# Optimization experiments

Hardware: AMD Instinct MI355X
Metric: run time of the kernel (lower is better)

The kernel has to match this reference:

```python
import jax, jax.numpy as jnp
import numpy as np

NUM_CLASSES = 250
NUM_EMB = 128
EMB_DIM = 512
HID = 256
IN_DIM = 225
COMMIT = 0.25


def _lstm_dir(x, Wih, Whh, b, reverse):
    # x: [B, T, D]; Wih: [4H, D]; Whh: [4H, H]; b: [4H]
    B = x.shape[0]
    H = Whh.shape[1]
    xs = jnp.swapaxes(x, 0, 1)            # [T, B, D]
    pre = xs @ Wih.T + b                   # precompute input projection: [T, B, 4H]

    def step(carry, pre_t):
        h, c = carry
        g = pre_t + h @ Whh.T
        i, f, gg, o = jnp.split(g, 4, axis=-1)  # torch gate order i,f,g,o
        i = jax.nn.sigmoid(i)
        f = jax.nn.sigmoid(f)
        gg = jnp.tanh(gg)
        o = jax.nn.sigmoid(o)
        c = f * c + i * gg
        h = o * jnp.tanh(c)
        return (h, c), h

    init = (jnp.zeros((B, H), x.dtype), jnp.zeros((B, H), x.dtype))
    _, hs = jax.lax.scan(step, init, pre, reverse=reverse)
    return jnp.swapaxes(hs, 0, 1)          # [B, T, H]


def _bilstm(x, Wih_f, Whh_f, b_f, Wih_b, Whh_b, b_b):
    hf = _lstm_dir(x, Wih_f, Whh_f, b_f, reverse=False)
    hb = _lstm_dir(x, Wih_b, Whh_b, b_b, reverse=True)
    return jnp.concatenate([hf, hb], axis=-1)  # [B, T, 2H]


def _vq(z, codebook):
    flat = z.reshape(-1, codebook.shape[1])  # [N, E]
    d = (jnp.sum(flat ** 2, axis=1, keepdims=True)
         + jnp.sum(codebook ** 2, axis=1)
         - 2.0 * flat @ codebook.T)          # [N, K]
    idx = jnp.argmin(d, axis=1)              # [N]
    q = codebook[idx].reshape(z.shape)
    e_loss = jnp.mean((jax.lax.stop_gradient(q) - z) ** 2)
    q_loss = jnp.mean((q - jax.lax.stop_gradient(z)) ** 2)
    loss = q_loss + COMMIT * e_loss
    q_st = z + jax.lax.stop_gradient(q - z)  # straight-through
    return q_st, loss


def setup_inputs() -> dict:
    key = jax.random.key(0)
    ks = jax.random.split(key, 16)
    s = 0.05
    d = {
        'x': jax.random.normal(ks[0], (64, 512, IN_DIM), dtype=jnp.float32),
        'enc_Wih_f': jax.random.normal(ks[1], (4 * HID, IN_DIM), jnp.float32) * s,
        'enc_Whh_f': jax.random.normal(ks[2], (4 * HID, HID), jnp.float32) * s,
        'enc_b_f': jnp.zeros((4 * HID,), jnp.float32),
        'enc_Wih_b': jax.random.normal(ks[3], (4 * HID, IN_DIM), jnp.float32) * s,
        'enc_Whh_b': jax.random.normal(ks[4], (4 * HID, HID), jnp.float32) * s,
        'enc_b_b': jnp.zeros((4 * HID,), jnp.float32),
        'codebook': jax.random.uniform(ks[5], (NUM_EMB, EMB_DIM), jnp.float32,
                                       minval=-1.0 / NUM_EMB, maxval=1.0 / NUM_EMB),
        'dec_Wih_f': jax.random.normal(ks[6], (4 * HID, EMB_DIM), jnp.float32) * s,
        'dec_Whh_f': jax.random.normal(ks[7], (4 * HID, HID), jnp.float32) * s,
        'dec_b_f': jnp.zeros((4 * HID,), jnp.float32),
        'dec_Wih_b': jax.random.normal(ks[8], (4 * HID, EMB_DIM), jnp.float32) * s,
        'dec_Whh_b': jax.random.normal(ks[9], (4 * HID, HID), jnp.float32) * s,
        'dec_b_b': jnp.zeros((4 * HID,), jnp.float32),
        'W_cls': jax.random.normal(ks[10], (NUM_CLASSES, EMB_DIM), jnp.float32) * s,
        'b_cls': jnp.zeros((NUM_CLASSES,), jnp.float32),
    }
    return d


def reference(x, enc_Wih_f, enc_Whh_f, enc_b_f, enc_Wih_b, enc_Whh_b, enc_b_b,
              codebook, dec_Wih_f, dec_Whh_f, dec_b_f, dec_Wih_b, dec_Whh_b, dec_b_b,
              W_cls, b_cls):
    enc_out = _bilstm(x, enc_Wih_f, enc_Whh_f, enc_b_f, enc_Wih_b, enc_Whh_b, enc_b_b)  # [B,T,512]
    quantized, vq_loss = _vq(enc_out, codebook)
    dec_out = _bilstm(quantized, dec_Wih_f, dec_Whh_f, dec_b_f, dec_Wih_b, dec_Whh_b, dec_b_b)
    logits = dec_out[:, -1] @ W_cls.T + b_cls  # [B, num_classes]
    return logits, vq_loss
```

## Files before the change

### kernel.cpp

```cpp
#include <hip/hip_runtime.h>
#include <hip/hip_fp16.h>
#include <cstddef>

#define Bb 64
#define Tt 512
#define INRAW 225
#define Hh 256
#define G4 1024
#define Ee 512
#define NCODE 128
#define NCLS 250

typedef _Float16 half8_t __attribute__((ext_vector_type(8)));
typedef float f32x4 __attribute__((ext_vector_type(4)));
typedef unsigned u32x4 __attribute__((ext_vector_type(4)));

__device__ __forceinline__ float sigf(float x) { return 1.0f / (1.0f + expf(-x)); }
__device__ __forceinline__ float fsig(float x) { return __builtin_amdgcn_rcpf(1.0f + __expf(-x)); }
__device__ __forceinline__ float ftanh(float x) {
  return 2.0f * __builtin_amdgcn_rcpf(1.0f + __expf(-2.0f * x)) - 1.0f;
}

__device__ __forceinline__ unsigned pkmax16(unsigned a, unsigned b) {
  unsigned r;
  asm("v_pk_max_i16 %0, %1, %2" : "=v"(r) : "v"(a), "v"(b));
  return r;
}

__global__ __launch_bounds__(256) void prep_all_k(
    u32x4* __restrict__ hexfill, const float* __restrict__ x, _Float16* __restrict__ xh,
    const float* __restrict__ dWihB, float* __restrict__ wpkbd,
    const float* __restrict__ eWhhF, _Float16* __restrict__ wphF,
    const float* __restrict__ eWhhB, _Float16* __restrict__ wphB,
    const float* __restrict__ dWhhF, _Float16* __restrict__ wphD,
    const float* __restrict__ eWihF, _Float16* __restrict__ wpihF,
    const float* __restrict__ eWihB, _Float16* __restrict__ wpihB,
    const float* __restrict__ dWihF, _Float16* __restrict__ wpihD) {
  int blk = blockIdx.x;
  const int tid = threadIdx.x;

  if (blk < 24576) {
    long i = (long)blk * 256 + tid;
    u32x4 v = {0x7C007C00u, 0x7C007C00u, 0x7C007C00u, 0x7C007C00u};
    asm volatile("global_store_dwordx4 %0, %1, off sc0 sc1"
                 :: "v"(hexfill + i), "v"(v) : "memory");
    return;
  }
  blk -= 24576;
  if (blk < 32768) {
    int idx = blk * 256 + tid;
    int row = idx >> 8, k = idx & 255;
    xh[idx] = (k < INRAW) ? (_Float16)x[(size_t)row * INRAW + k] : (_Float16)0.f;
    return;
  }
  blk -= 32768;
  if (blk < 2048) {
    int idx = blk * 256 + tid;
    int jg = idx >> 9;
    int k = idx & 511;
    int j = jg >> 2, g = jg & 3;
    wpkbd[(((size_t)k << 8) + j) * 4 + g] = dWihB[(size_t)(g * 256 + j) * 512 + k];
    return;
  }
  blk -= 2048;
  if (blk < 3072) {
    const float* W = (blk < 1024) ? eWhhF : (blk < 2048) ? eWhhB : dWhhF;
    _Float16* wp = (blk < 1024) ? wphF : (blk < 2048) ? wphB : wphD;
    int idx = (blk & 1023) * 256 + tid;
    int e = idx & 7, l = (idx >> 3) & 63, zg = (idx >> 9) & 7;
    int ks = (idx >> 12) & 7, wv = (idx >> 15) & 7;
    int z = zg >> 2, g = zg & 3;
    int u = wv * 32 + z * 16 + (l & 15);
    int k = ks * 32 + (l >> 4) * 8 + e;
    wp[idx] = (_Float16)W[(size_t)(g * 256 + u) * 256 + k];
    return;
  }
  blk -= 3072;
  if (blk < 2048) {
    const float* W = (blk < 1024) ? eWihF : eWihB;
    _Float16* wp = (blk < 1024) ? wpihF : wpihB;
    int idx = (blk & 1023) * 256 + tid;
    int e = idx & 7, l = (idx >> 3) & 63;
    int tail = idx >> 9;
    int ks = tail & 7; tail >>= 3;
    int z = tail & 1, w = (tail >> 1) & 7, g = tail >> 4;
    if (g >= 4) return;
    int k = ks * 32 + (l >> 4) * 8 + e;
    int u = w * 32 + z * 16 + (l & 15);
    wp[idx] = (k < INRAW) ? (_Float16)W[(size_t)(g * 256 + u) * INRAW + k] : (_Float16)0.f;
    return;
  }
  blk -= 2048;
  {
    int idx = blk * 256 + tid;
    int e = idx & 7, l = (idx >> 3) & 63;
    int tail = idx >> 9;
    int ks = tail & 15; tail >>= 4;
    int z = tail & 1, w = (tail >> 1) & 7, g = tail >> 4;
    if (g >= 4) return;
    int k = ks * 32 + (l >> 4) * 8 + e;
    int u = w * 32 + z * 16 + (l & 15);
    wpihD[idx] = (_Float16)dWihF[(size_t)(g * 256 + u) * 512 + k];
  }
}

__global__ __launch_bounds__(256) void gemm_mfma_pre(const _Float16* __restrict__ Ah,
                                                     const _Float16* __restrict__ Bp0,
                                                     const float* __restrict__ bias0,
                                                     __half* __restrict__ C0,
                                                     const _Float16* __restrict__ Bp1,
                                                     const float* __restrict__ bias1,
                                                     __half* __restrict__ C1, int K) {
  const int t = blockIdx.x, g = blockIdx.y;
  const int zsel = blockIdx.z;
  const _Float16* Bp = zsel ? Bp1 : Bp0;
  const float* bias = zsel ? bias1 : bias0;
  __half* C = zsel ? C1 : C0;
  const int bg = threadIdx.x >> 6;
  const int l = threadIdx.x & 63, l15 = l & 15, lg = l >> 4;
  const int KS = K >> 5;

  f32x4 acc[16];
#pragma unroll
  for (int ct = 0; ct < 16; ++ct) acc[ct] = (f32x4){0.f, 0.f, 0.f, 0.f};

  const _Float16* arow = Ah + ((size_t)(bg * 16 + l15) * 512 + t) * K + lg * 8;

  for (int kh = 0; kh < KS; kh += 8) {
    half8_t af[8];
#pragma unroll
    for (int k2 = 0; k2 < 8; ++k2)
      af[k2] = *(const half8_t*)(arow + (kh + k2) * 32);
#pragma unroll
    for (int ct = 0; ct < 16; ++ct) {
      const int w = ct >> 1, z = ct & 1;
      const _Float16* bb = Bp + ((((size_t)(g * 8 + w) * 2 + z) * KS + kh) * 64 + l) * 8;
#pragma unroll
      for (int k2 = 0; k2 < 8; ++k2) {
        half8_t bf = *(const half8_t*)(bb + (size_t)k2 * 512);
        acc[ct] = __builtin_amdgcn_mfma_f32_16x16x32_f16(af[k2], bf, acc[ct], 0, 0, 0);
      }
    }
  }

#pragma unroll
  for (int ct = 0; ct < 16; ++ct) {
    const int w = ct >> 1, z = ct & 1;
    const int u = w * 32 + z * 16 + l15;
    const float bs = bias[g * 256 + u];
    union { unsigned short us[4]; uint2 u2; } pk;
#pragma unroll
    for (int j = 0; j < 4; ++j) {
      __half hv = __float2half(acc[ct][j] + bs);
      pk.us[j] = *(unsigned short*)&hv;
    }
    __half* dst = C + ((((size_t)t * 4 + bg) * 8 + w) * 2 + z) * 1024 + l * 16 + g * 4;
    *(uint2*)dst = pk.u2;
  }
}

__global__ __launch_bounds__(64) void lstm_scan_sync(
    const half8_t* __restrict__ preF, const half8_t* __restrict__ wF,
    _Float16* __restrict__ hexF,
    const half8_t* __restrict__ preB, const half8_t* __restrict__ wB,
    _Float16* __restrict__ hexB, int nfwd) {
  const int isB = (blockIdx.x >= nfwd) ? 1 : 0;
  const half8_t* pre = isB ? preB : preF;
  const half8_t* wfrag = isB ? wB : wF;
  _Float16* hex = isB ? hexB : hexF;
  const int bid = blockIdx.x - (isB ? nfwd : 0);
  const int rg = bid >> 4, sl = bid & 15;
  const int w_ = sl >> 1, z_ = sl & 1;
  const int l = threadIdx.x, l15 = l & 15, lg = l >> 4;
  const int u0 = sl * 16;

  half8_t bfr[8][4];
#pragma unroll
  for (int ks = 0; ks < 8; ++ks)
#pragma unroll
    for (int g = 0; g < 4; ++g)
      bfr[ks][g] = wfrag[(size_t)((w_ * 8 + ks) * 8 + z_ * 4 + g) * 64 + l];

  float c[4] = {0.f, 0.f, 0.f, 0.f};
  half8_t pc0, pc1;
  {
    const int t0 = isB ? (Tt - 1) : 0;
    const half8_t* pp = pre + ((size_t)(t0 * 4 + rg) * 16 + sl) * 128 + l * 2;
    pc0 = pp[0]; pc1 = pp[1];
  }

  for (int s = 0; s < Tt; ++s) {
    f32x4 acc[4];
#pragma unroll
    for (int g = 0; g < 4; ++g)
#pragma unroll
      for (int j = 0; j < 4; ++j)
        acc[g][j] = (float)((g < 2 ? pc0 : pc1)[(g & 1) * 4 + j]);

    if (s + 1 < Tt) {
      const int tn = isB ? (Tt - 2 - s) : (s + 1);
      const half8_t* pp = pre + ((size_t)(tn * 4 + rg) * 16 + sl) * 128 + l * 2;
      pc0 = pp[0]; pc1 = pp[1];
    }

    if (s > 0) {
      const char* ab = (const char*)hex + (((size_t)(s - 1) * 64 + rg * 16) * 256) * 2;
      half8_t afr[8];
      while (true) {
#pragma unroll
        for (int ks = 0; ks < 8; ++ks) {
          const void* ap = (const void*)(ab + l15 * 512 + ks * 64 + lg * 16);
          asm volatile("global_load_dwordx4 %0, %1, off sc0 sc1"
                       : "=v"(afr[ks]) : "v"(ap) : "memory");
        }
        asm volatile("s_waitcnt vmcnt(0)" ::: "memory");
        union HU { half8_t h; u32x4 u; } cu;
        cu.h = afr[0];
        unsigned mm = pkmax16(pkmax16(cu.u[0], cu.u[1]), pkmax16(cu.u[2], cu.u[3]));
#pragma unroll
        for (int ks = 1; ks < 8; ++ks) {
          cu.h = afr[ks];
          mm = pkmax16(mm, pkmax16(pkmax16(cu.u[0], cu.u[1]), pkmax16(cu.u[2], cu.u[3])));
        }
        int bad = ((mm & 0xFFFFu) == 0x7C00u) || ((mm >> 16) == 0x7C00u);
        if (__all(!bad)) break;
      }
      __builtin_amdgcn_sched_barrier(0);

#pragma unroll
      for (int ks = 0; ks < 8; ++ks)
#pragma unroll
        for (int g = 0; g < 4; ++g)
          acc[g] = __builtin_amdgcn_mfma_f32_16x16x32_f16(afr[ks], bfr[ks][g], acc[g], 0, 0, 0);
    }

#pragma unroll
    for (int j = 0; j < 4; ++j) {
      float iv = fsig(acc[0][j]);
      float fv = fsig(acc[1][j]);
      float gv = ftanh(acc[2][j]);
      float ov = fsig(acc[3][j]);
      c[j] = fv * c[j] + iv * gv;
      float hv = ov * ftanh(c[j]);
      union { _Float16 f; unsigned short u; } cv;
      cv.f = (_Float16)hv;
      unsigned hb32 = cv.u;
      const void* hp = (const void*)(hex + ((size_t)s * 64 + rg * 16 + lg * 4 + j) * 256
                                     + u0 + l15);
      asm volatile("global_store_short %0, %1, off sc0 sc1"
                   :: "v"(hp), "v"(hb32) : "memory");
    }
  }
}

#define VPB 4
__global__ __launch_bounds__(128) void vq_kernel(const _Float16* __restrict__ hexF,
                                                 const _Float16* __restrict__ hexB,
                                                 const float* __restrict__ cb,
                                                 _Float16* __restrict__ qh,
                                                 float* __restrict__ dmin) {
  const int tid = threadIdx.x;
  const int v0 = blockIdx.x * VPB;
  __shared__ __align__(16) float zs[VPB][Ee];
  __shared__ float dsh[NCODE];
  __shared__ int ish[NCODE];
  __shared__ int best[VPB];

#pragma unroll
  for (int v = 0; v < VPB; ++v) {
    const int vv = v0 + v;
    const int b = vv >> 9, t = vv & 511;
    const _Float16* hf = hexF + ((size_t)t * 64 + b) * 256;
    const _Float16* hb = hexB + ((size_t)(Tt - 1 - t) * 64 + b) * 256;
    zs[v][tid]       = (float)hf[tid];
    zs[v][tid + 128] = (float)hf[tid + 128];
    zs[v][tid + 256] = (float)hb[tid];
    zs[v][tid + 384] = (float)hb[tid + 128];
  }
  __syncthreads();

  float dv[VPB] = {0.0f, 0.0f, 0.0f, 0.0f};
  const float4* crow = (const float4*)(cb + (size_t)tid * Ee);
#pragma unroll 2
  for (int e4 = 0; e4 < Ee / 4; ++e4) {
    float4 cc = crow[e4];
#pragma unroll
    for (int v = 0; v < VPB; ++v) {
      float4 z = *(const float4*)&zs[v][e4 * 4];
      float t0 = z.x - cc.x, t1 = z.y - cc.y, t2 = z.z - cc.z, t3 = z.w - cc.w;
      dv[v] = fmaf(t0, t0, dv[v]);
      dv[v] = fmaf(t1, t1, dv[v]);
      dv[v] = fmaf(t2, t2, dv[v]);
      dv[v] = fmaf(t3, t3, dv[v]);
    }
  }

#pragma unroll
  for (int v = 0; v < VPB; ++v) {
    __syncthreads();
    dsh[tid] = dv[v];
    ish[tid] = tid;
    __syncthreads();
    for (int off = 64; off > 0; off >>= 1) {
      if (tid < off) {
        float dn = dsh[tid + off];
        int in_ = ish[tid + off];
        if (dn < dsh[tid] || (dn == dsh[tid] && in_ < ish[tid])) {
          dsh[tid] = dn;
          ish[tid] = in_;
        }
      }
      __syncthreads();
    }
    if (tid == 0) {
      best[v] = ish[0];
      dmin[v0 + v] = dsh[0];
    }
  }
  __syncthreads();

#pragma unroll
  for (int v = 0; v < VPB; ++v) {
    const float* cbest = cb + (size_t)best[v] * Ee;
    _Float16* qrow = qh + (size_t)(v0 + v) * Ee;
#pragma unroll
    for (int u = 0; u < 4; ++u) {
      int e = tid + u * 128;
      float z = zs[v][e];
      qrow[e] = (_Float16)(z + (cbest[e] - z));
    }
  }
}

__global__ __launch_bounds__(1024) void vq_reduce(const float* __restrict__ dmin,
                                                  float* __restrict__ out) {
  __shared__ float sh[1024];
  int tid = threadIdx.x;
  float s = 0.0f;
  for (int i = tid; i < Bb * Tt; i += 1024) s += dmin[i];
  sh[tid] = s;
  __syncthreads();
  for (int off = 512; off > 0; off >>= 1) {
    if (tid < off) sh[tid] += sh[tid + off];
    __syncthreads();
  }
  if (tid == 0) out[Bb * NCLS] = sh[0] * (1.25f / ((float)(Bb * Tt) * (float)Ee));
}

__global__ __launch_bounds__(256) void dec_bwd_last(const _Float16* __restrict__ qh,
                                                    const float* __restrict__ wpB,
                                                    const float* __restrict__ bias,
                                                    float* __restrict__ hb_last) {
  int b = blockIdx.x, tid = threadIdx.x;
  __shared__ __align__(16) float zsl[Ee];
  const _Float16* qrow = qh + ((size_t)b * Tt + (Tt - 1)) * Ee;
  zsl[tid] = (float)qrow[tid];
  zsl[tid + 256] = (float)qrow[tid + 256];
  __syncthreads();
  float a0 = bias[tid], a1 = bias[256 + tid], a2 = bias[512 + tid], a3 = bias[768 + tid];
  const float4* wp4 = (const float4*)wpB;
#pragma unroll 4
  for (int k = 0; k < Ee; ++k) {
    float zk = zsl[k];
    float4 w = wp4[((size_t)k << 8) + tid];
    a0 = fmaf(zk, w.x, a0); a1 = fmaf(zk, w.y, a1);
    a2 = fmaf(zk, w.z, a2); a3 = fmaf(zk, w.w, a3);
  }
  float i = sigf(a0), f = sigf(a1), g = tanhf(a2), o = sigf(a3);
  (void)f;
  float cc = i * g;
  hb_last[b * Hh + tid] = o * tanhf(cc);
}

__global__ __launch_bounds__(256) void classifier_k(const _Float16* __restrict__ hexD,
                                                    const float* __restrict__ hb_last,
                                                    const float* __restrict__ Wcls,
                                                    const float* __restrict__ bcls,
                                                    float* __restrict__ out) {
  int b = blockIdx.x, tid = threadIdx.x;
  __shared__ __align__(16) float dl[Ee];
  dl[tid] = (float)hexD[((size_t)(Tt - 1) * 64 + b) * 256 + tid];
  dl[tid + 256] = hb_last[b * Hh + tid];
  __syncthreads();
  if (tid < NCLS) {
    const float4* wr = (const float4*)(Wcls + (size_t)tid * Ee);
    float acc = bcls[tid];
#pragma unroll 4
    for (int e4 = 0; e4 < Ee / 4; ++e4) {
      float4 w = wr[e4];
      float4 z = *(const float4*)&dl[e4 * 4];
      acc = fmaf(w.x, z.x, acc);
      acc = fmaf(w.y, z.y, acc);
      acc = fmaf(w.z, z.z, acc);
      acc = fmaf(w.w, z.w, acc);
    }
    out[b * NCLS + tid] = acc;
  }
}

extern "C" void kernel_launch(void* const* d_in, const int* in_sizes, int n_in,
                              void* d_out, int out_size, void* d_ws, size_t ws_size,
                              hipStream_t stream) {
  const float* x     = (const float*)d_in[0];
  const float* eWihF = (const float*)d_in[1];
  const float* eWhhF = (const float*)d_in[2];
  const float* ebF   = (const float*)d_in[3];
  const float* eWihB = (const float*)d_in[4];
  const float* eWhhB = (const float*)d_in[5];
  const float* ebB   = (const float*)d_in[6];
  const float* cb    = (const float*)d_in[7];
  const float* dWihF = (const float*)d_in[8];
  const float* dWhhF = (const float*)d_in[9];
  const float* dbF   = (const float*)d_in[10];
  const float* dWihB = (const float*)d_in[11];
  const float* dbB   = (const float*)d_in[13];
  const float* Wcls  = (const float*)d_in[14];
  const float* bcls  = (const float*)d_in[15];
  float* out = (float*)d_out;
  float* w = (float*)d_ws;

  const size_t MR = (size_t)Bb * Tt;
  const size_t SZ_PRE_H = MR * G4 / 2;
  const size_t SZ_HEX  = (size_t)Tt * Bb * Hh / 2;
  const size_t SZ_XH   = MR * 256 / 2;
  const size_t SZ_WPK  = (size_t)512 * G4;
  const size_t SZ_WPH  = (size_t)G4 * Hh / 2;
  const size_t SZ_WIH  = (size_t)4 * 8 * 2 * 8 * 64 * 8 / 2;
  const size_t SZ_WIHD = SZ_WIH * 2;

  size_t o = 0;
  __half* preFh = (__half*)(w + o); o += SZ_PRE_H;
  __half* preBh = (__half*)(w + o); o += SZ_PRE_H;
  _Float16* hexF = (_Float16*)(w + o); o += SZ_HEX;
  _Float16* hexB = (_Float16*)(w + o); o += SZ_HEX;
  _Float16* hexD = (_Float16*)(w + o); o += SZ_HEX;
  _Float16* xh = (_Float16*)(w + o); o += SZ_XH;
  float* wpkbd = w + o; o += SZ_WPK;
  _Float16* wphF = (_Float16*)(w + o); o += SZ_WPH;
  _Float16* wphB = (_Float16*)(w + o); o += SZ_WPH;
  _Float16* wphD = (_Float16*)(w + o); o += SZ_WPH;
  _Float16* wpihF = (_Float16*)(w + o); o += SZ_WIH;
  _Float16* wpihB = (_Float16*)(w + o); o += SZ_WIH;
  _Float16* wpihD = (_Float16*)(w + o); o += SZ_WIHD;
  float* dminp = w + o; o += MR;
  float* hbl   = w + o; o += (size_t)Bb * Hh;
  _Float16* qh = (_Float16*)preFh;
  __half* dprf = preBh;

  hipLaunchKernelGGL(prep_all_k, dim3(66560), dim3(256), 0, stream,
                     (u32x4*)hexF, x, xh,
                     dWihB, wpkbd,
                     eWhhF, wphF, eWhhB, wphB, dWhhF, wphD,
                     eWihF, wpihF, eWihB, wpihB, dWihF, wpihD);

  hipLaunchKernelGGL(gemm_mfma_pre, dim3(Tt, 4, 2), dim3(256), 0, stream,
                     xh, wpihF, ebF, preFh, wpihB, ebB, preBh, 256);

  hipLaunchKernelGGL(lstm_scan_sync, dim3(128), dim3(64), 0, stream,
                     (const half8_t*)preFh, (const half8_t*)wphF, hexF,
                     (const half8_t*)preBh, (const half8_t*)wphB, hexB, 64);

  hipLaunchKernelGGL(vq_kernel, dim3((int)(MR / VPB)), dim3(128), 0, stream,
                     hexF, hexB, cb, qh, dminp);
  hipLaunchKernelGGL(vq_reduce, dim3(1), dim3(1024), 0, stream, dminp, out);

  hipLaunchKernelGGL(gemm_mfma_pre, dim3(Tt, 4, 1), dim3(256), 0, stream,
                     qh, wpihD, dbF, dprf, wpihD, dbF, dprf, 512);

  hipLaunchKernelGGL(dec_bwd_last, dim3(Bb), dim3(256), 0, stream, qh, wpkbd, dbB, hbl);

  hipLaunchKernelGGL(lstm_scan_sync, dim3(64), dim3(64), 0, stream,
                     (const half8_t*)dprf, (const half8_t*)wphD, hexD,
                     (const half8_t*)dprf, (const half8_t*)wphD, hexD, 64);

  hipLaunchKernelGGL(classifier_k, dim3(Bb), dim3(256), 0, stream,
                     hexD, hbl, Wcls, bcls, out);
}
```

Baseline: 2.545 ms.

## Poll local L2 mirror for LSTM hidden-state exchange with system-scope fallback

The recurrent scan now writes each hidden state twice: to an L2-scoped buffer (sc0 only) and to the coherent global buffer (sc0 sc1). Consumers poll the cheaper L2-scoped copy a few times before falling back to the fully coherent copy. Blocks are remapped so the eight row groups of one slice are interleaved by blockIdx, which is intended to place cooperating blocks on the same XCD and L2. The cost is extra stores, extra inf-fill kernels for the mirror buffers, and reliance on an assumed block-to-XCD placement.

Result: slower. 2.863 ms (+12.5%).

```diff
diff --git a/kernel.cpp b/kernel.cpp
--- a/kernel.cpp
+++ b/kernel.cpp
@@ -27,8 +27,18 @@
   return r;
 }
 
+__global__ __launch_bounds__(256) void fill_inf4_k(u32x4* __restrict__ p, long n4) {
+  long i = (long)blockIdx.x * 256 + threadIdx.x;
+  const long stride = (long)gridDim.x * 256;
+  u32x4 v = {0x7C007C00u, 0x7C007C00u, 0x7C007C00u, 0x7C007C00u};
+  for (; i < n4; i += stride) {
+    asm volatile("global_store_dwordx4 %0, %1, off sc0 sc1" :: "v"(p + i), "v"(v) : "memory");
+  }
+}
+
 __global__ __launch_bounds__(256) void prep_all_k(
-    u32x4* __restrict__ hexfill, const float* __restrict__ x, _Float16* __restrict__ xh,
+    u32x4* __restrict__ hexfill, u32x4* __restrict__ hexblfill,
+    const float* __restrict__ x, _Float16* __restrict__ xh,
     const float* __restrict__ dWihB, float* __restrict__ wpkbd,
     const float* __restrict__ eWhhF, _Float16* __restrict__ wphF,
     const float* __restrict__ eWhhB, _Float16* __restrict__ wphB,
@@ -38,15 +48,22 @@
     const float* __restrict__ dWihF, _Float16* __restrict__ wpihD) {
   int blk = blockIdx.x;
   const int tid = threadIdx.x;
-
-  if (blk < 24576) {
+  u32x4 sv = {0x7C007C00u, 0x7C007C00u, 0x7C007C00u, 0x7C007C00u};
+
+  if (blk < 12288) {
     long i = (long)blk * 256 + tid;
-    u32x4 v = {0x7C007C00u, 0x7C007C00u, 0x7C007C00u, 0x7C007C00u};
     asm volatile("global_store_dwordx4 %0, %1, off sc0 sc1"
-                 :: "v"(hexfill + i), "v"(v) : "memory");
+                 :: "v"(hexfill + i), "v"(sv) : "memory");
     return;
   }
-  blk -= 24576;
+  blk -= 12288;
+  if (blk < 4096) {
+    long i = (long)blk * 256 + tid;
+    asm volatile("global_store_dwordx4 %0, %1, off sc0 sc1"
+                 :: "v"(hexblfill + i), "v"(sv) : "memory");
+    return;
+  }
+  blk -= 4096;
   if (blk < 32768) {
     int idx = blk * 256 + tid;
     int row = idx >> 8, k = idx & 255;
@@ -161,15 +178,19 @@
 
 __global__ __launch_bounds__(64) void lstm_scan_sync(
     const half8_t* __restrict__ preF, const half8_t* __restrict__ wF,
-    _Float16* __restrict__ hexF,
+    _Float16* __restrict__ hexgF, _Float16* __restrict__ hexlF,
     const half8_t* __restrict__ preB, const half8_t* __restrict__ wB,
-    _Float16* __restrict__ hexB, int nfwd) {
-  const int isB = (blockIdx.x >= nfwd) ? 1 : 0;
+    _Float16* __restrict__ hexgB, _Float16* __restrict__ hexlB,
+    int ngTot) {
+  const int group = blockIdx.x & 7;
+  const int sl = blockIdx.x >> 3;
+  if (group >= ngTot) return;
+  const int isB = (group >= 4) ? 1 : 0;
+  const int rg = group & 3;
   const half8_t* pre = isB ? preB : preF;
   const half8_t* wfrag = isB ? wB : wF;
-  _Float16* hex = isB ? hexB : hexF;
-  const int bid = blockIdx.x - (isB ? nfwd : 0);
-  const int rg = bid >> 4, sl = bid & 15;
+  _Float16* hexg = isB ? hexgB : hexgF;
+  _Float16* hexl = isB ? hexlB : hexlF;
   const int w_ = sl >> 1, z_ = sl & 1;
   const int l = threadIdx.x, l15 = l & 15, lg = l >> 4;
   const int u0 = sl * 16;
@@ -204,13 +225,16 @@
     }
 
     if (s > 0) {
-      const char* ab = (const char*)hex + (((size_t)(s - 1) * 64 + rg * 16) * 256) * 2;
+      const size_t boff = (((size_t)(s - 1) * 64 + rg * 16) * 256) * 2;
+      const char* abl = (const char*)hexl + boff;
+      const char* abg = (const char*)hexg + boff;
       half8_t afr[8];
-      while (true) {
+      int ok = 0;
+      for (int tr = 0; tr < 4; ++tr) {
 #pragma unroll
         for (int ks = 0; ks < 8; ++ks) {
-          const void* ap = (const void*)(ab + l15 * 512 + ks * 64 + lg * 16);
-          asm volatile("global_load_dwordx4 %0, %1, off sc0 sc1"
+          const void* ap = (const void*)(abl + l15 * 512 + ks * 64 + lg * 16);
+          asm volatile("global_load_dwordx4 %0, %1, off sc0"
                        : "=v"(afr[ks]) : "v"(ap) : "memory");
         }
         asm volatile("s_waitcnt vmcnt(0)" ::: "memory");
@@ -223,7 +247,28 @@
           mm = pkmax16(mm, pkmax16(pkmax16(cu.u[0], cu.u[1]), pkmax16(cu.u[2], cu.u[3])));
         }
         int bad = ((mm & 0xFFFFu) == 0x7C00u) || ((mm >> 16) == 0x7C00u);
-        if (__all(!bad)) break;
+        if (__all(!bad)) { ok = 1; break; }
+      }
+      if (!ok) {
+        while (true) {
+#pragma unroll
+          for (int ks = 0; ks < 8; ++ks) {
+            const void* ap = (const void*)(abg + l15 * 512 + ks * 64 + lg * 16);
+            asm volatile("global_load_dwordx4 %0, %1, off sc0 sc1"
+                         : "=v"(afr[ks]) : "v"(ap) : "memory");
+          }
+          asm volatile("s_waitcnt vmcnt(0)" ::: "memory");
+          union HU { half8_t h; u32x4 u; } cu;
+          cu.h = afr[0];
+          unsigned mm = pkmax16(pkmax16(cu.u[0], cu.u[1]), pkmax16(cu.u[2], cu.u[3]));
+#pragma unroll
+          for (int ks = 1; ks < 8; ++ks) {
+            cu.h = afr[ks];
+            mm = pkmax16(mm, pkmax16(pkmax16(cu.u[0], cu.u[1]), pkmax16(cu.u[2], cu.u[3])));
+          }
+          int bad = ((mm & 0xFFFFu) == 0x7C00u) || ((mm >> 16) == 0x7C00u);
+          if (__all(!bad)) break;
+        }
       }
       __builtin_amdgcn_sched_barrier(0);
 
@@ -245,10 +290,11 @@
       union { _Float16 f; unsigned short u; } cv;
       cv.f = (_Float16)hv;
       unsigned hb32 = cv.u;
-      const void* hp = (const void*)(hex + ((size_t)s * 64 + rg * 16 + lg * 4 + j) * 256
-                                     + u0 + l15);
+      const size_t hidx = ((size_t)s * 64 + rg * 16 + lg * 4 + j) * 256 + u0 + l15;
+      asm volatile("global_store_short %0, %1, off sc0"
+                   :: "v"((const void*)(hexl + hidx)), "v"(hb32) : "memory");
       asm volatile("global_store_short %0, %1, off sc0 sc1"
-                   :: "v"(hp), "v"(hb32) : "memory");
+                   :: "v"((const void*)(hexg + hidx)), "v"(hb32) : "memory");
     }
   }
 }
@@ -435,6 +481,7 @@
   _Float16* hexB = (_Float16*)(w + o); o += SZ_HEX;
   _Float16* hexD = (_Float16*)(w + o); o += SZ_HEX;
   _Float16* xh = (_Float16*)(w + o); o += SZ_XH;
+  _Float16* hexBl = (_Float16*)(w + o); o += SZ_HEX;
   float* wpkbd = w + o; o += SZ_WPK;
   _Float16* wphF = (_Float16*)(w + o); o += SZ_WPH;
   _Float16* wphB = (_Float16*)(w + o); o += SZ_WPH;
@@ -446,9 +493,11 @@
   float* hbl   = w + o; o += (size_t)Bb * Hh;
   _Float16* qh = (_Float16*)preFh;
   __half* dprf = preBh;
-
-  hipLaunchKernelGGL(prep_all_k, dim3(66560), dim3(256), 0, stream,
-                     (u32x4*)hexF, x, xh,
+  _Float16* hexFl = xh;
+  _Float16* hexDl = hexBl;
+
+  hipLaunchKernelGGL(prep_all_k, dim3(58368), dim3(256), 0, stream,
+                     (u32x4*)hexF, (u32x4*)hexBl, x, xh,
                      dWihB, wpkbd,
                      eWhhF, wphF, eWhhB, wphB, dWhhF, wphD,
                      eWihF, wpihF, eWihB, wpihB, dWihF, wpihD);
@@ -456,22 +505,28 @@
   hipLaunchKernelGGL(gemm_mfma_pre, dim3(Tt, 4, 2), dim3(256), 0, stream,
                      xh, wpihF, ebF, preFh, wpihB, ebB, preBh, 256);
 
+  hipLaunchKernelGGL(fill_inf4_k, dim3(2048), dim3(256), 0, stream,
+                     (u32x4*)hexFl, (long)(SZ_HEX / 4));
+
   hipLaunchKernelGGL(lstm_scan_sync, dim3(128), dim3(64), 0, stream,
-                     (const half8_t*)preFh, (const half8_t*)wphF, hexF,
-                     (const half8_t*)preBh, (const half8_t*)wphB, hexB, 64);
+                     (const half8_t*)preFh, (const half8_t*)wphF, hexF, hexFl,
+                     (const half8_t*)preBh, (const half8_t*)wphB, hexB, hexBl, 8);
 
   hipLaunchKernelGGL(vq_kernel, dim3((int)(MR / VPB)), dim3(128), 0, stream,
                      hexF, hexB, cb, qh, dminp);
   hipLaunchKernelGGL(vq_reduce, dim3(1), dim3(1024), 0, stream, dminp, out);
 
+  hipLaunchKernelGGL(fill_inf4_k, dim3(2048), dim3(256), 0, stream,
+                     (u32x4*)hexDl, (long)(SZ_HEX / 4));
+
   hipLaunchKernelGGL(gemm_mfma_pre, dim3(Tt, 4, 1), dim3(256), 0, stream,
                      qh, wpihD, dbF, dprf, wpihD, dbF, dprf, 512);
 
   hipLaunchKernelGGL(dec_bwd_last, dim3(Bb), dim3(256), 0, stream, qh, wpkbd, dbB, hbl);
 
-  hipLaunchKernelGGL(lstm_scan_sync, dim3(64), dim3(64), 0, stream,
-                     (const half8_t*)dprf, (const half8_t*)wphD, hexD,
-                     (const half8_t*)dprf, (const half8_t*)wphD, hexD, 64);
+  hipLaunchKernelGGL(lstm_scan_sync, dim3(128), dim3(64), 0, stream,
+                     (const half8_t*)dprf, (const half8_t*)wphD, hexD, hexDl,
+                     (const half8_t*)dprf, (const half8_t*)wphD, hexD, hexDl, 4);
 
   hipLaunchKernelGGL(classifier_k, dim3(Bb), dim3(256), 0, stream,
                      hexD, hbl, Wcls, bcls, out);
```

## Precompute codebook projections and gather decoder inputs by VQ index

Applied to the files above, without the earlier changes.

The decoder input is always one of 128 codebook rows, so the decoder input projection (codebook times Wih plus bias) is computed once per code in the prep kernel. The full 32768x512x1024 decoder GEMM and the quantized-tensor write are replaced by a gather from that table keyed on the VQ argmin index. The backward-direction last-step projection becomes a table lookup as well. The hex fill region is halved, presumably because hexD no longer needs the sentinel fill. Results now use the exact codebook row rather than the straight-through z+(q-z) value rounded to fp16, so numerics differ slightly.

After: 2.399 ms, median of 2. 1.06x faster.

```diff
diff --git a/kernel.cpp b/kernel.cpp
--- a/kernel.cpp
+++ b/kernel.cpp
@@ -12,6 +12,7 @@
 #define NCLS 250
 
 typedef _Float16 half8_t __attribute__((ext_vector_type(8)));
+typedef _Float16 half4_t __attribute__((ext_vector_type(4)));
 typedef float f32x4 __attribute__((ext_vector_type(4)));
 typedef unsigned u32x4 __attribute__((ext_vector_type(4)));
 
@@ -28,25 +29,29 @@
 }
 
 __global__ __launch_bounds__(256) void prep_all_k(
-    u32x4* __restrict__ hexfill, const float* __restrict__ x, _Float16* __restrict__ xh,
-    const float* __restrict__ dWihB, float* __restrict__ wpkbd,
+    u32x4* __restrict__ hexfill,
+    const float* __restrict__ x, _Float16* __restrict__ xh,
+    const float* __restrict__ cb,
+    const float* __restrict__ dWihF, const float* __restrict__ dbF,
+    _Float16* __restrict__ projFh,
+    const float* __restrict__ dWihB, const float* __restrict__ dbB,
+    float* __restrict__ projBf,
     const float* __restrict__ eWhhF, _Float16* __restrict__ wphF,
     const float* __restrict__ eWhhB, _Float16* __restrict__ wphB,
     const float* __restrict__ dWhhF, _Float16* __restrict__ wphD,
     const float* __restrict__ eWihF, _Float16* __restrict__ wpihF,
-    const float* __restrict__ eWihB, _Float16* __restrict__ wpihB,
-    const float* __restrict__ dWihF, _Float16* __restrict__ wpihD) {
+    const float* __restrict__ eWihB, _Float16* __restrict__ wpihB) {
   int blk = blockIdx.x;
   const int tid = threadIdx.x;
 
-  if (blk < 24576) {
+  if (blk < 12288) {
     long i = (long)blk * 256 + tid;
-    u32x4 v = {0x7C007C00u, 0x7C007C00u, 0x7C007C00u, 0x7C007C00u};
+    u32x4 sv = {0x7C007C00u, 0x7C007C00u, 0x7C007C00u, 0x7C007C00u};
     asm volatile("global_store_dwordx4 %0, %1, off sc0 sc1"
-                 :: "v"(hexfill + i), "v"(v) : "memory");
+                 :: "v"(hexfill + i), "v"(sv) : "memory");
     return;
   }
-  blk -= 24576;
+  blk -= 12288;
   if (blk < 32768) {
     int idx = blk * 256 + tid;
     int row = idx >> 8, k = idx & 255;
@@ -54,15 +59,39 @@
     return;
   }
   blk -= 32768;
-  if (blk < 2048) {
-    int idx = blk * 256 + tid;
-    int jg = idx >> 9;
-    int k = idx & 511;
-    int j = jg >> 2, g = jg & 3;
-    wpkbd[(((size_t)k << 8) + j) * 4 + g] = dWihB[(size_t)(g * 256 + j) * 512 + k];
+  if (blk < 512) {
+    int n = (blk & 3) * 256 + tid;
+    int code = blk >> 2;
+    const float4* cr = (const float4*)(cb + (size_t)code * Ee);
+    const float4* wr = (const float4*)(dWihF + (size_t)n * Ee);
+    float acc = 0.f;
+#pragma unroll 4
+    for (int e4 = 0; e4 < Ee / 4; ++e4) {
+      float4 cv = cr[e4], wv = wr[e4];
+      acc = fmaf(cv.x, wv.x, acc); acc = fmaf(cv.y, wv.y, acc);
+      acc = fmaf(cv.z, wv.z, acc); acc = fmaf(cv.w, wv.w, acc);
+    }
+    int g = n >> 8, u = n & 255;
+    projFh[(size_t)code * 1024 + u * 4 + g] = (_Float16)(acc + dbF[n]);
     return;
   }
-  blk -= 2048;
+  blk -= 512;
+  if (blk < 512) {
+    int n = (blk & 3) * 256 + tid;
+    int code = blk >> 2;
+    const float4* cr = (const float4*)(cb + (size_t)code * Ee);
+    const float4* wr = (const float4*)(dWihB + (size_t)n * Ee);
+    float acc = 0.f;
+#pragma unroll 4
+    for (int e4 = 0; e4 < Ee / 4; ++e4) {
+      float4 cv = cr[e4], wv = wr[e4];
+      acc = fmaf(cv.x, wv.x, acc); acc = fmaf(cv.y, wv.y, acc);
+      acc = fmaf(cv.z, wv.z, acc); acc = fmaf(cv.w, wv.w, acc);
+    }
+    projBf[(size_t)code * 1024 + n] = acc + dbB[n];
+    return;
+  }
+  blk -= 512;
   if (blk < 3072) {
     const float* W = (blk < 1024) ? eWhhF : (blk < 2048) ? eWhhB : dWhhF;
     _Float16* wp = (blk < 1024) ? wphF : (blk < 2048) ? wphB : wphD;
@@ -76,7 +105,7 @@
     return;
   }
   blk -= 3072;
-  if (blk < 2048) {
+  {
     const float* W = (blk < 1024) ? eWihF : eWihB;
     _Float16* wp = (blk < 1024) ? wpihF : wpihB;
     int idx = (blk & 1023) * 256 + tid;
@@ -88,19 +117,6 @@
     int k = ks * 32 + (l >> 4) * 8 + e;
     int u = w * 32 + z * 16 + (l & 15);
     wp[idx] = (k < INRAW) ? (_Float16)W[(size_t)(g * 256 + u) * INRAW + k] : (_Float16)0.f;
-    return;
-  }
-  blk -= 2048;
-  {
-    int idx = blk * 256 + tid;
-    int e = idx & 7, l = (idx >> 3) & 63;
-    int tail = idx >> 9;
-    int ks = tail & 15; tail >>= 4;
-    int z = tail & 1, w = (tail >> 1) & 7, g = tail >> 4;
-    if (g >= 4) return;
-    int k = ks * 32 + (l >> 4) * 8 + e;
-    int u = w * 32 + z * 16 + (l & 15);
-    wpihD[idx] = (_Float16)dWihF[(size_t)(g * 256 + u) * 512 + k];
   }
 }
 
@@ -257,14 +273,13 @@
 __global__ __launch_bounds__(128) void vq_kernel(const _Float16* __restrict__ hexF,
                                                  const _Float16* __restrict__ hexB,
                                                  const float* __restrict__ cb,
-                                                 _Float16* __restrict__ qh,
+                                                 int* __restrict__ idxOut,
                                                  float* __restrict__ dmin) {
   const int tid = threadIdx.x;
   const int v0 = blockIdx.x * VPB;
   __shared__ __align__(16) float zs[VPB][Ee];
   __shared__ float dsh[NCODE];
   __shared__ int ish[NCODE];
-  __shared__ int best[VPB];
 
 #pragma unroll
   for (int v = 0; v < VPB; ++v) {
@@ -313,21 +328,42 @@
       __syncthreads();
     }
     if (tid == 0) {
-      best[v] = ish[0];
+      idxOut[v0 + v] = ish[0];
       dmin[v0 + v] = dsh[0];
     }
   }
-  __syncthreads();
-
-#pragma unroll
-  for (int v = 0; v < VPB; ++v) {
-    const float* cbest = cb + (size_t)best[v] * Ee;
-    _Float16* qrow = qh + (size_t)(v0 + v) * Ee;
-#pragma unroll
-    for (int u = 0; u < 4; ++u) {
-      int e = tid + u * 128;
-      float z = zs[v][e];
-      qrow[e] = (_Float16)(z + (cbest[e] - z));
+}
+
+__global__ __launch_bounds__(256) void gather_pre_k(const int* __restrict__ idx,
+                                                    const _Float16* __restrict__ projFh,
+                                                    __half* __restrict__ C) {
+  const int t = blockIdx.x;
+  const int b_ = threadIdx.x >> 6;
+  const int l = threadIdx.x & 63, l15 = l & 15, lg = l >> 4;
+
+  int cj[4];
+#pragma unroll
+  for (int j = 0; j < 4; ++j)
+    cj[j] = idx[(size_t)(b_ * 16 + lg * 4 + j) * 512 + t];
+
+#pragma unroll
+  for (int w_ = 0; w_ < 8; ++w_) {
+#pragma unroll
+    for (int z_ = 0; z_ < 2; ++z_) {
+      const int u = w_ * 32 + z_ * 16 + l15;
+      half4_t pv[4];
+#pragma unroll
+      for (int j = 0; j < 4; ++j)
+        pv[j] = *(const half4_t*)(projFh + (size_t)cj[j] * 1024 + u * 4);
+      union { _Float16 h[16]; u32x4 q[2]; } outv;
+#pragma unroll
+      for (int g = 0; g < 4; ++g)
+#pragma unroll
+        for (int j = 0; j < 4; ++j)
+          outv.h[g * 4 + j] = pv[j][g];
+      __half* dst = C + ((((size_t)t * 4 + b_) * 8 + w_) * 2 + z_) * 1024 + l * 16;
+      *(u32x4*)dst = outv.q[0];
+      *(u32x4*)(dst + 8) = outv.q[1];
     }
   }
 }
@@ -347,25 +383,13 @@
   if (tid == 0) out[Bb * NCLS] = sh[0] * (1.25f / ((float)(Bb * Tt) * (float)Ee));
 }
 
-__global__ __launch_bounds__(256) void dec_bwd_last(const _Float16* __restrict__ qh,
-                                                    const float* __restrict__ wpB,
-                                                    const float* __restrict__ bias,
+__global__ __launch_bounds__(256) void dec_bwd_last(const int* __restrict__ idx,
+                                                    const float* __restrict__ projBf,
                                                     float* __restrict__ hb_last) {
   int b = blockIdx.x, tid = threadIdx.x;
-  __shared__ __align__(16) float zsl[Ee];
-  const _Float16* qrow = qh + ((size_t)b * Tt + (Tt - 1)) * Ee;
-  zsl[tid] = (float)qrow[tid];
-  zsl[tid + 256] = (float)qrow[tid + 256];
-  __syncthreads();
-  float a0 = bias[tid], a1 = bias[256 + tid], a2 = bias[512 + tid], a3 = bias[768 + tid];
-  const float4* wp4 = (const float4*)wpB;
-#pragma unroll 4
-  for (int k = 0; k < Ee; ++k) {
-    float zk = zsl[k];
-    float4 w = wp4[((size_t)k << 8) + tid];
-    a0 = fmaf(zk, w.x, a0); a1 = fmaf(zk, w.y, a1);
-    a2 = fmaf(zk, w.z, a2); a3 = fmaf(zk, w.w, a3);
-  }
+  const int c = idx[(size_t)b * 512 + 511];
+  const float* pr = projBf + (size_t)c * 1024;
+  float a0 = pr[tid], a1 = pr[256 + tid], a2 = pr[512 + tid], a3 = pr[768 + tid];
   float i = sigf(a0), f = sigf(a1), g = tanhf(a2), o = sigf(a3);
   (void)f;
   float cc = i * g;
@@ -423,10 +447,10 @@
   const size_t SZ_PRE_H = MR * G4 / 2;
   const size_t SZ_HEX  = (size_t)Tt * Bb * Hh / 2;
   const size_t SZ_XH   = MR * 256 / 2;
-  const size_t SZ_WPK  = (size_t)512 * G4;
   const size_t SZ_WPH  = (size_t)G4 * Hh / 2;
   const size_t SZ_WIH  = (size_t)4 * 8 * 2 * 8 * 64 * 8 / 2;
-  const size_t SZ_WIHD = SZ_WIH * 2;
+  const size_t SZ_PJF  = (size_t)NCODE * G4 / 2;
+  const size_t SZ_PJB  = (size_t)NCODE * G4;
 
   size_t o = 0;
   __half* preFh = (__half*)(w + o); o += SZ_PRE_H;
@@ -435,23 +459,23 @@
   _Float16* hexB = (_Float16*)(w + o); o += SZ_HEX;
   _Float16* hexD = (_Float16*)(w + o); o += SZ_HEX;
   _Float16* xh = (_Float16*)(w + o); o += SZ_XH;
-  float* wpkbd = w + o; o += SZ_WPK;
   _Float16* wphF = (_Float16*)(w + o); o += SZ_WPH;
   _Float16* wphB = (_Float16*)(w + o); o += SZ_WPH;
   _Float16* wphD = (_Float16*)(w + o); o += SZ_WPH;
   _Float16* wpihF = (_Float16*)(w + o); o += SZ_WIH;
   _Float16* wpihB = (_Float16*)(w + o); o += SZ_WIH;
-  _Float16* wpihD = (_Float16*)(w + o); o += SZ_WIHD;
+  _Float16* projFh = (_Float16*)(w + o); o += SZ_PJF;
+  float* projBf = w + o; o += SZ_PJB;
+  int* idxp = (int*)(w + o); o += MR;
   float* dminp = w + o; o += MR;
   float* hbl   = w + o; o += (size_t)Bb * Hh;
-  _Float16* qh = (_Float16*)preFh;
   __half* dprf = preBh;
 
-  hipLaunchKernelGGL(prep_all_k, dim3(66560), dim3(256), 0, stream,
+  hipLaunchKernelGGL(prep_all_k, dim3(51200), dim3(256), 0, stream,
                      (u32x4*)hexF, x, xh,
-                     dWihB, wpkbd,
+                     cb, dWihF, dbF, projFh, dWihB, dbB, projBf,
                      eWhhF, wphF, eWhhB, wphB, dWhhF, wphD,
-                     eWihF, wpihF, eWihB, wpihB, dWihF, wpihD);
+                     eWihF, wpihF, eWihB, wpihB);
 
   hipLaunchKernelGGL(gemm_mfma_pre, dim3(Tt, 4, 2), dim3(256), 0, stream,
                      xh, wpihF, ebF, preFh, wpihB, ebB, preBh, 256);
@@ -461,13 +485,13 @@
                      (const half8_t*)preBh, (const half8_t*)wphB, hexB, 64);
 
   hipLaunchKernelGGL(vq_kernel, dim3((int)(MR / VPB)), dim3(128), 0, stream,
-                     hexF, hexB, cb, qh, dminp);
+                     hexF, hexB, cb, idxp, dminp);
   hipLaunchKernelGGL(vq_reduce, dim3(1), dim3(1024), 0, stream, dminp, out);
 
-  hipLaunchKernelGGL(gemm_mfma_pre, dim3(Tt, 4, 1), dim3(256), 0, stream,
-                     qh, wpihD, dbF, dprf, wpihD, dbF, dprf, 512);
-
-  hipLaunchKernelGGL(dec_bwd_last, dim3(Bb), dim3(256), 0, stream, qh, wpkbd, dbB, hbl);
+  hipLaunchKernelGGL(gather_pre_k, dim3(Tt), dim3(256), 0, stream,
+                     idxp, projFh, dprf);
+
+  hipLaunchKernelGGL(dec_bwd_last, dim3(Bb), dim3(256), 0, stream, idxp, projBf, hbl);
 
   hipLaunchKernelGGL(lstm_scan_sync, dim3(64), dim3(64), 0, stream,
                      (const half8_t*)dprf, (const half8_t*)wphD, hexD,
```
